# Optimization experiments

Measured on AMD Instinct MI355X. Metric: run time of the kernel, lower is better.

The kernel has to match this reference:

```python
import jax, jax.numpy as jnp
import numpy as np

R = 0.01          # slice width (init kwarg r)
DIM = 0           # init kwarg dim = 'x'
NUM_SLICES = 101  # static bound: coords ~ U[0,1) so ceil(range/R) <= 100; +1 safety


def setup_inputs() -> dict:
    key = jax.random.key(0)
    k1, k2 = jax.random.split(key)
    B, N = 16, 65536
    x = jax.random.uniform(k1, (B, 3, N), dtype=jnp.float32)      # point coords in [0,1)
    x_64 = jax.random.normal(k2, (B, 64, N), dtype=jnp.float32)   # per-point features
    return {"x": x, "x_64": x_64, "batch_": B, "points": N}


def reference(x, x_64, batch_, points):
    # per-batch min along the chosen axis: [B]
    pmin = x[:, DIM, :].min(axis=1)
    coord = x[:, DIM, :]                                          # [B, N]
    # bucket index per point (torch.floor((point - min)/r))
    k = jnp.floor((coord - pmin[:, None]) / R).astype(jnp.int32)  # [B, N]
    seg = k.reshape(-1)                                           # [B*N] global slice ids (original pools across batch)
    feats = jnp.transpose(x_64, (0, 2, 1)).reshape(-1, 64)        # [B*N, 64]
    # vectorized segment max replacing the python per-slice loop
    max_feature = jax.ops.segment_max(feats, seg, num_segments=NUM_SLICES)  # [NUM_SLICES, 64]
    counts = jax.ops.segment_sum(jnp.ones_like(seg, dtype=jnp.int32), seg,
                                 num_segments=NUM_SLICES)         # [NUM_SLICES] = slice_num
    return max_feature, counts
```

## Files before the change

kernel.cpp:

```cpp
#include <hip/hip_runtime.h>

#define NSEG 101
#define NCH 64
#define NPTS 65536
#define NBATCH 16
#define NMAX (NCH * NSEG)
#define NOUT (NMAX + NSEG)
#define FLT_BIG 3.4028234663852886e38f

#define SENT 0x007FFFFFu
#define BITS_EMPTY 0xFF7F0000u
#define BITS_POS_CLAMP 0x7F7F0000u

static __device__ __forceinline__ unsigned enc(float f) {
    unsigned b = (unsigned)__float_as_int(f);
    return b ^ (0x80000000u | (unsigned)((int)b >> 31));
}
static __device__ __forceinline__ unsigned dec_bits(unsigned u) {
    unsigned flip = (u & 0x80000000u) ? 0x80000000u : 0xFFFFFFFFu;
    return u ^ flip;
}

__global__ void sp2_seed(unsigned* __restrict__ acc) {
    int e = blockIdx.x * 256 + threadIdx.x;
    if (e < NMAX) acc[e] = SENT;
    else if (e < NOUT) acc[e] = 0u;
}

__global__ __launch_bounds__(1024) void sp2_main(const float* __restrict__ x,
                                                 const float* __restrict__ x64,
                                                 unsigned* __restrict__ acc) {
    __shared__ unsigned smax[NMAX];
    __shared__ unsigned scnt[NSEG];
    __shared__ float swmin[16];
    int t = threadIdx.x;
    for (int i = t; i < NMAX; i += 1024) smax[i] = SENT;
    if (t < NSEG) scnt[t] = 0u;

    int b = blockIdx.x >> 5;
    int chunk = blockIdx.x & 31;

    const float4* crow = (const float4*)(x + (size_t)b * 3 * NPTS);
    float m = FLT_BIG;
    #pragma unroll
    for (int i = 0; i < 16; i++) {
        float4 v = crow[t + i * 1024];
        m = fminf(m, fminf(fminf(v.x, v.y), fminf(v.z, v.w)));
    }
    #pragma unroll
    for (int off = 32; off; off >>= 1)
        m = fminf(m, __shfl_down(m, off, 64));
    if ((t & 63) == 0) swmin[t >> 6] = m;
    __syncthreads();
    float pm = swmin[0];
    #pragma unroll
    for (int i = 1; i < 16; i++) pm = fminf(pm, swmin[i]);

    int n0 = chunk * 2048 + t * 2;
    float2 cv = *(const float2*)(x + (size_t)b * 3 * NPTS + n0);
    int k0 = (int)floorf((cv.x - pm) / 0.01f);
    int k1 = (int)floorf((cv.y - pm) / 0.01f);
    k0 = k0 < 0 ? 0 : (k0 > NSEG - 1 ? NSEG - 1 : k0);
    k1 = k1 < 0 ? 0 : (k1 > NSEG - 1 ? NSEG - 1 : k1);
    atomicAdd(&scnt[k0], 1u);
    atomicAdd(&scnt[k1], 1u);

    const float* gp = x64 + (size_t)b * NCH * NPTS + n0;
    #pragma unroll 4
    for (int c = 0; c < NCH; c++) {
        float2 v = *(const float2*)gp;
        atomicMax(&smax[c * NSEG + k0], enc(v.x));
        atomicMax(&smax[c * NSEG + k1], enc(v.y));
        gp += NPTS;
    }
    __syncthreads();

    for (int e = t; e < NOUT; e += 1024) {
        if (e < NMAX) {
            unsigned v = smax[(e & 63) * NSEG + (e >> 6)];
            if (v != SENT) atomicMax(&acc[e], v);
        } else {
            unsigned v = scnt[e - NMAX];
            if (v) atomicAdd(&acc[e], v);
        }
    }
}

__global__ void sp2_fin(unsigned* __restrict__ acc) {
    int e = blockIdx.x * 256 + threadIdx.x;
    if (e >= NOUT) return;
    unsigned u = acc[e];
    unsigned ob;
    if (e < NMAX) {
        if (u == SENT) {
            ob = BITS_EMPTY;
        } else {
            ob = dec_bits(u);
            unsigned mag = ob & 0x7FFFFFFFu;
            if (mag >= 0x7F7F8000u)
                ob = (ob & 0x80000000u) | BITS_POS_CLAMP;
        }
    } else {
        ob = (unsigned)__float_as_int((float)u);
    }
    acc[e] = ob;
}

extern "C" void kernel_launch(void* const* d_in, const int* in_sizes, int n_in,
                              void* d_out, int out_size, void* d_ws, size_t ws_size,
                              hipStream_t stream) {
    const float* x   = (const float*)d_in[0];
    const float* x64 = (const float*)d_in[1];
    unsigned* acc = (unsigned*)d_out;
    (void)d_ws; (void)ws_size; (void)in_sizes; (void)n_in; (void)out_size;

    sp2_seed<<<(NOUT + 255) / 256, 256, 0, stream>>>(acc);
    sp2_main<<<NBATCH * 32, 1024, 0, stream>>>(x, x64, acc);
    sp2_fin<<<(NOUT + 255) / 256, 256, 0, stream>>>(acc);
}
```

Before: 70.54 us.

## Hoist per-batch min into separate kernel and widen main kernel to float4 loads

Moves the per-batch coordinate-min reduction out of the main kernel into a small kernel that writes 16 mins to workspace, so the 512 main blocks no longer each re-read the whole coordinate row. The main kernel now uses 512 threads each handling 4 points with float4 loads and a deeper unroll. This trades one extra launch and a dependency for removing redundant global reads, and keeps a fallback that recomputes the min when no workspace is available.

```diff
diff --git a/kernel.cpp b/kernel.cpp
--- a/kernel.cpp
+++ b/kernel.cpp
@@ -21,25 +21,15 @@
     return u ^ flip;
 }
 
-__global__ void sp2_seed(unsigned* __restrict__ acc) {
+__global__ void sp3_seed(unsigned* __restrict__ acc) {
     int e = blockIdx.x * 256 + threadIdx.x;
     if (e < NMAX) acc[e] = SENT;
     else if (e < NOUT) acc[e] = 0u;
 }
 
-__global__ __launch_bounds__(1024) void sp2_main(const float* __restrict__ x,
-                                                 const float* __restrict__ x64,
-                                                 unsigned* __restrict__ acc) {
-    __shared__ unsigned smax[NMAX];
-    __shared__ unsigned scnt[NSEG];
-    __shared__ float swmin[16];
-    int t = threadIdx.x;
-    for (int i = t; i < NMAX; i += 1024) smax[i] = SENT;
-    if (t < NSEG) scnt[t] = 0u;
-
-    int b = blockIdx.x >> 5;
-    int chunk = blockIdx.x & 31;
-
+__global__ __launch_bounds__(1024) void sp3_min(const float* __restrict__ x,
+                                                float* __restrict__ pmins) {
+    int b = blockIdx.x, t = threadIdx.x;
     const float4* crow = (const float4*)(x + (size_t)b * 3 * NPTS);
     float m = FLT_BIG;
     #pragma unroll
@@ -50,32 +40,81 @@
     #pragma unroll
     for (int off = 32; off; off >>= 1)
         m = fminf(m, __shfl_down(m, off, 64));
-    if ((t & 63) == 0) swmin[t >> 6] = m;
+    __shared__ float sm[16];
+    if ((t & 63) == 0) sm[t >> 6] = m;
     __syncthreads();
-    float pm = swmin[0];
-    #pragma unroll
-    for (int i = 1; i < 16; i++) pm = fminf(pm, swmin[i]);
+    if (t == 0) {
+        float r = sm[0];
+        #pragma unroll
+        for (int i = 1; i < 16; i++) r = fminf(r, sm[i]);
+        pmins[b] = r;
+    }
+}
 
-    int n0 = chunk * 2048 + t * 2;
-    float2 cv = *(const float2*)(x + (size_t)b * 3 * NPTS + n0);
+template<bool PMIN_WS>
+__global__ __launch_bounds__(512) void sp3_main(const float* __restrict__ x,
+                                                const float* __restrict__ x64,
+                                                const float* __restrict__ pmins,
+                                                unsigned* __restrict__ acc) {
+    __shared__ unsigned smax[NMAX];
+    __shared__ unsigned scnt[NSEG];
+    int t = threadIdx.x;
+    for (int i = t; i < NMAX; i += 512) smax[i] = SENT;
+    if (t < NSEG) scnt[t] = 0u;
+
+    int b = blockIdx.x >> 5;
+    int chunk = blockIdx.x & 31;
+
+    float pm;
+    if constexpr (PMIN_WS) {
+        pm = pmins[b];
+        __syncthreads();
+    } else {
+        __shared__ float swmin[8];
+        const float4* crow = (const float4*)(x + (size_t)b * 3 * NPTS);
+        float m = FLT_BIG;
+        #pragma unroll
+        for (int i = 0; i < 32; i++) {
+            float4 v = crow[t + i * 512];
+            m = fminf(m, fminf(fminf(v.x, v.y), fminf(v.z, v.w)));
+        }
+        #pragma unroll
+        for (int off = 32; off; off >>= 1)
+            m = fminf(m, __shfl_down(m, off, 64));
+        if ((t & 63) == 0) swmin[t >> 6] = m;
+        __syncthreads();
+        pm = swmin[0];
+        #pragma unroll
+        for (int i = 1; i < 8; i++) pm = fminf(pm, swmin[i]);
+    }
+
+    int n0 = chunk * 2048 + t * 4;
+    float4 cv = *(const float4*)(x + (size_t)b * 3 * NPTS + n0);
     int k0 = (int)floorf((cv.x - pm) / 0.01f);
     int k1 = (int)floorf((cv.y - pm) / 0.01f);
+    int k2 = (int)floorf((cv.z - pm) / 0.01f);
+    int k3 = (int)floorf((cv.w - pm) / 0.01f);
     k0 = k0 < 0 ? 0 : (k0 > NSEG - 1 ? NSEG - 1 : k0);
     k1 = k1 < 0 ? 0 : (k1 > NSEG - 1 ? NSEG - 1 : k1);
+    k2 = k2 < 0 ? 0 : (k2 > NSEG - 1 ? NSEG - 1 : k2);
+    k3 = k3 < 0 ? 0 : (k3 > NSEG - 1 ? NSEG - 1 : k3);
     atomicAdd(&scnt[k0], 1u);
     atomicAdd(&scnt[k1], 1u);
+    atomicAdd(&scnt[k2], 1u);
+    atomicAdd(&scnt[k3], 1u);
 
     const float* gp = x64 + (size_t)b * NCH * NPTS + n0;
-    #pragma unroll 4
+    #pragma unroll 8
     for (int c = 0; c < NCH; c++) {
-        float2 v = *(const float2*)gp;
+        float4 v = *(const float4*)(gp + (size_t)c * NPTS);
         atomicMax(&smax[c * NSEG + k0], enc(v.x));
         atomicMax(&smax[c * NSEG + k1], enc(v.y));
-        gp += NPTS;
+        atomicMax(&smax[c * NSEG + k2], enc(v.z));
+        atomicMax(&smax[c * NSEG + k3], enc(v.w));
     }
     __syncthreads();
 
-    for (int e = t; e < NOUT; e += 1024) {
+    for (int e = t; e < NOUT; e += 512) {
         if (e < NMAX) {
             unsigned v = smax[(e & 63) * NSEG + (e >> 6)];
             if (v != SENT) atomicMax(&acc[e], v);
@@ -86,7 +125,7 @@
     }
 }
 
-__global__ void sp2_fin(unsigned* __restrict__ acc) {
+__global__ void sp3_fin(unsigned* __restrict__ acc) {
     int e = blockIdx.x * 256 + threadIdx.x;
     if (e >= NOUT) return;
     unsigned u = acc[e];
@@ -112,9 +151,14 @@
     const float* x   = (const float*)d_in[0];
     const float* x64 = (const float*)d_in[1];
     unsigned* acc = (unsigned*)d_out;
-    (void)d_ws; (void)ws_size; (void)in_sizes; (void)n_in; (void)out_size;
+    float* pmins = (float*)d_ws;
 
-    sp2_seed<<<(NOUT + 255) / 256, 256, 0, stream>>>(acc);
-    sp2_main<<<NBATCH * 32, 1024, 0, stream>>>(x, x64, acc);
-    sp2_fin<<<(NOUT + 255) / 256, 256, 0, stream>>>(acc);
+    sp3_seed<<<(NOUT + 255) / 256, 256, 0, stream>>>(acc);
+    if (ws_size >= NBATCH * sizeof(float)) {
+        sp3_min<<<NBATCH, 1024, 0, stream>>>(x, pmins);
+        sp3_main<true><<<NBATCH * 32, 512, 0, stream>>>(x, x64, pmins, acc);
+    } else {
+        sp3_main<false><<<NBATCH * 32, 512, 0, stream>>>(x, x64, nullptr, acc);
+    }
+    sp3_fin<<<(NOUT + 255) / 256, 256, 0, stream>>>(acc);
 }
```

Measured after the change: 63.19 us. -10.4%, faster.
